# Kernel optimization log

Measured on AMD Instinct MI355X. Metric: run time of the kernel, lower is better.

The kernel has to match this reference:

```python
import jax, jax.numpy as jnp
import numpy as np

N = 8192      # number of input points
K = 16        # nsample for all kNN groupings
STRIDE = 4    # TransitionDown stride -> M = N // 4 output points


def _knn(q, p, k):
    # squared euclidean distances [m, n] -> k nearest indices per query
    d2 = jnp.sum(q * q, 1)[:, None] + jnp.sum(p * p, 1)[None, :] - 2.0 * (q @ p.T)
    return jax.lax.top_k(-d2, k)[1]


def _forward(points, We1, se1, be1, We2, se2, be2,
             Wq1, Wk1, Wv1, sa1, ba1, Wq2, Wk2, Wv2, sa2, ba2,
             Wtd, sd, bd, Wu1, su1, bu1, Wu2, su2, bu2,
             Wc1, bc1, sc, bc, Wc2, bc2):
    p = points[0]                      # [N, 3]
    n = p.shape[0]
    idx = _knn(p, p, K)                # [N, K] shared xyz-kNN (same coords every layer)

    def edge_conv(x, W, s, b):
        # DGCNN EdgeConv: concat(x_i, x_j - x_i) -> Linear -> BN(affine) -> ReLU -> max_k
        xi = x[:, None, :]
        xj = x[idx]                    # [N, K, C]
        e = jnp.concatenate([jnp.broadcast_to(xi, xj.shape), xj - xi], -1)
        h = jax.nn.relu((e @ W) * s + b)
        return h.max(axis=1)

    def graph_attn(x, Wq, Wk, Wv, s, b):
        q, kk, v = x @ Wq, x @ Wk, x @ Wv
        kj, vj = kk[idx], v[idx]       # [N, K, D]
        logits = jnp.einsum('nd,nkd->nk', q, kj) / jnp.sqrt(jnp.float32(q.shape[-1]))
        a = jax.nn.softmax(logits, axis=-1)
        y = jnp.einsum('nk,nkd->nd', a, vj)
        return jax.nn.relu(y * s + b)

    x = edge_conv(p, We1, se1, be1)            # 3 -> 64
    x = edge_conv(x, We2, se2, be2)            # 64 -> 128
    x = graph_attn(x, Wq1, Wk1, Wv1, sa1, ba1) # 128 -> 256
    x = graph_attn(x, Wq2, Wk2, Wv2, sa2, ba2) # 256 -> 512

    # TransitionDown: subsample n/stride points, group kNN with relative xyz, MLP, max-pool
    sel = jnp.arange(0, n, STRIDE)
    pm = p[sel]                                 # [M, 3]
    idx_d = _knn(pm, p, K)                      # [M, K]
    g = jnp.concatenate([p[idx_d] - pm[:, None, :], x[idx_d]], -1)  # [M, K, 3+512]
    xd = jax.nn.relu((g @ Wtd) * sd + bd).max(axis=1)               # [M, 512]

    # TransitionUp(x, o): local linear + broadcast per-cloud pooled branch (single cloud, o=[n])
    gmean = xd.mean(axis=0, keepdims=True)
    xu = jax.nn.relu((xd @ Wu1) * su1 + bu1 + (gmean @ Wu2) * su2 + bu2)  # [M, 256]

    # classifier (eval mode: dropout = identity, BN folded to affine)
    h = jax.nn.relu(((xu @ Wc1) + bc1) * sc + bc)
    return h @ Wc2 + bc2               # [M, num_classes]


def setup_inputs() -> dict:
    key = jax.random.key(0)
    ks = iter(jax.random.split(key, 64))
    def w(shape):
        return jax.random.normal(next(ks), shape, jnp.float32) / jnp.sqrt(jnp.float32(shape[0]))
    def s(d):
        return 1.0 + 0.01 * jax.random.normal(next(ks), (d,), jnp.float32)
    def b(d):
        return 0.01 * jax.random.normal(next(ks), (d,), jnp.float32)
    return {
        'points': jax.random.normal(next(ks), (1, N, 3), jnp.float32),
        'We1': w((6, 64)), 'se1': s(64), 'be1': b(64),
        'We2': w((128, 128)), 'se2': s(128), 'be2': b(128),
        'Wq1': w((128, 256)), 'Wk1': w((128, 256)), 'Wv1': w((128, 256)), 'sa1': s(256), 'ba1': b(256),
        'Wq2': w((256, 512)), 'Wk2': w((256, 512)), 'Wv2': w((256, 512)), 'sa2': s(512), 'ba2': b(512),
        'Wtd': w((515, 512)), 'sd': s(512), 'bd': b(512),
        'Wu1': w((512, 256)), 'su1': s(256), 'bu1': b(256),
        'Wu2': w((512, 256)), 'su2': s(256), 'bu2': b(256),
        'Wc1': w((256, 128)), 'bc1': b(128), 'sc': s(128), 'bc': b(128),
        'Wc2': w((128, 6)), 'bc2': b(6),
    }


def reference(points, We1, se1, be1, We2, se2, be2,
              Wq1, Wk1, Wv1, sa1, ba1, Wq2, Wk2, Wv2, sa2, ba2,
              Wtd, sd, bd, Wu1, su1, bu1, Wu2, su2, bu2,
              Wc1, bc1, sc, bc, Wc2, bc2):
    return _forward(points, We1, se1, be1, We2, se2, be2,
                    Wq1, Wk1, Wv1, sa1, ba1, Wq2, Wk2, Wv2, sa2, ba2,
                    Wtd, sd, bd, Wu1, su1, bu1, Wu2, su2, bu2,
                    Wc1, bc1, sc, bc, Wc2, bc2)
```

## Files before the change

### kernel.cpp

```cpp
#include <hip/hip_runtime.h>


#define NP 8192
#define NDOWN 2048
#define KCAP 64

typedef unsigned long long u64;
typedef __attribute__((ext_vector_type(8))) _Float16 half8;
typedef __attribute__((ext_vector_type(4))) unsigned short us4;
typedef __attribute__((ext_vector_type(8))) unsigned short ushort8;
typedef __attribute__((ext_vector_type(4))) float f32x4;

__device__ __forceinline__ bool lexless(float ad, int ai, float bd, int bi) {
  return ad < bd || (ad == bd && ai < bi);
}

__device__ __forceinline__ unsigned short f2h(float x) {
  _Float16 h = (_Float16)x;
  return __builtin_bit_cast(unsigned short, h);
}
__device__ __forceinline__ float h2f(unsigned short u) {
  return (float)__builtin_bit_cast(_Float16, u);
}

__global__ __launch_bounds__(256) void prep_points_k(const float* __restrict__ pts,
                                                     float4* __restrict__ soa) {
  int i = blockIdx.x * 256 + threadIdx.x;
  float x = pts[3 * i], y = pts[3 * i + 1], z = pts[3 * i + 2];
  soa[i] = make_float4(x, y, z, x * x + y * y + z * z);
}

__global__ __launch_bounds__(256) void wsplit_k(
    const float* __restrict__ We2, const float* __restrict__ Wq1,
    const float* __restrict__ Wk1, const float* __restrict__ Wv1,
    const float* __restrict__ Wq2, const float* __restrict__ Wk2,
    const float* __restrict__ Wv2, const float* __restrict__ Wtd,
    const float* __restrict__ Wu1, const float* __restrict__ Wc1,
    unsigned short* __restrict__ whi) {
  int t = blockIdx.x * 256 + threadIdx.x;
  float v;
  if (t < 16384) {
    int n = t >> 6, k = t & 63;
    if (n < 128) v = We2[k * 128 + n] - We2[(k + 64) * 128 + n];
    else         v = We2[(k + 64) * 128 + (n - 128)];
  } else if (t < 114688) {
    int e = t - 16384;
    int n = e >> 7, k = e & 127;
    if (n < 256)      v = Wq1[k * 256 + n];
    else if (n < 512) v = Wk1[k * 256 + (n - 256)];
    else              v = Wv1[k * 256 + (n - 512)];
  } else if (t < 507904) {
    int e = t - 114688;
    int n = e >> 8, k = e & 255;
    if (n < 512)       v = Wq2[k * 512 + n];
    else if (n < 1024) v = Wk2[k * 512 + (n - 512)];
    else               v = Wv2[k * 512 + (n - 1024)];
  } else if (t < 770048) {
    int e = t - 507904;
    int n = e >> 9, k = e & 511;
    v = Wtd[(3 + k) * 512 + n];
  } else if (t < 901120) {
    int e = t - 770048;
    int n = e >> 9, k = e & 511;
    v = Wu1[k * 256 + n];
  } else {
    int e = t - 901120;
    int n = e >> 8, k = e & 255;
    v = Wc1[k * 128 + n];
  }
  whi[t] = f2h(v);
}

__device__ __forceinline__ void bitonic_val64(float& d, int lane) {
#pragma unroll
  for (int k = 2; k <= 64; k <<= 1) {
#pragma unroll
    for (int j = k >> 1; j >= 1; j >>= 1) {
      float od = __shfl_xor(d, j);
      bool takeMin = (((lane & k) == 0) == ((lane & j) == 0));
      d = takeMin ? fminf(d, od) : fmaxf(d, od);
    }
  }
}

__device__ __forceinline__ void bitonic_lex64(float& d, int& i, int lane) {
#pragma unroll
  for (int k = 2; k <= 64; k <<= 1) {
#pragma unroll
    for (int j = k >> 1; j >= 1; j >>= 1) {
      float od = __shfl_xor(d, j);
      int oi = __shfl_xor(i, j);
      bool takeMin = (((lane & k) == 0) == ((lane & j) == 0));
      bool less = lexless(od, oi, d, i);
      if (takeMin == less) { d = od; i = oi; }
    }
  }
}

__device__ __forceinline__ void insert1(float cd, int ci, int lane,
                                        float& td, int& ti) {
  int p = __popcll(__ballot(lexless(td, ti, cd, ci)));
  if (p < 16) {
    float ud = __shfl_up(td, 1);
    int ui = __shfl_up(ti, 1);
    float ntd = td; int nti = ti;
    if (lane > p && lane < 16) { ntd = ud; nti = ui; }
    if (lane == p) { ntd = cd; nti = ci; }
    td = ntd; ti = nti;
  }
}

__global__ __launch_bounds__(512) void knn_k(const float4* __restrict__ soa,
                                             int* __restrict__ idxout) {
  __shared__ float4 sp[2048];
  __shared__ float cb_d[8][KCAP];
  __shared__ int cb_i[8][KCAP];
  __shared__ int ccnt[8];
  const int lane = threadIdx.x & 63;
  const int wid = threadIdx.x >> 6;
  const int q = blockIdx.x * 8 + wid;
  const float4 qp = soa[q];
  const float qx2 = -2.f * qp.x, qy2 = -2.f * qp.y, qz2 = -2.f * qp.z;
  const float INF = __int_as_float(0x7f800000);
  if (lane == 0) ccnt[wid] = 0;

  float md = INF;
  for (int ch = 0; ch < 4; ++ch) {
    __syncthreads();
    for (int j = 0; j < 4; ++j) {
      int e = j * 512 + threadIdx.x;
      sp[e] = soa[ch * 2048 + e];
    }
    __syncthreads();
#pragma unroll 4
    for (int c = 0; c < 32; ++c) {
      const float4 P = sp[c * 64 + lane];
      float m = fmaf(qx2, P.x, qp.w);
      m = fmaf(qy2, P.y, m);
      m = fmaf(qz2, P.z, m);
      md = fminf(md, m + P.w);
    }
  }
  float sv = md;
  bitonic_val64(sv, lane);
  const float tau = __shfl(sv, 15);
  const float tauM = tau + fabsf(tau) * 1e-5f + 1e-12f;

  for (int ch = 0; ch < 4; ++ch) {
    __syncthreads();
    for (int j = 0; j < 4; ++j) {
      int e = j * 512 + threadIdx.x;
      sp[e] = soa[ch * 2048 + e];
    }
    __syncthreads();
#pragma unroll 4
    for (int c = 0; c < 32; ++c) {
      const float4 P = sp[c * 64 + lane];
      float m = fmaf(qx2, P.x, qp.w);
      m = fmaf(qy2, P.y, m);
      m = fmaf(qz2, P.z, m);
      const float d = m + P.w;
      if (d <= tauM) {
        int slot = atomicAdd(&ccnt[wid], 1);
        if (slot < KCAP) {
          cb_d[wid][slot] = d;
          cb_i[wid][slot] = ch * 2048 + c * 64 + lane;
        }
      }
    }
  }
  int n = ccnt[wid];
  if (n <= KCAP) {
    float dd = (lane < n) ? cb_d[wid][lane] : INF;
    int ii = (lane < n) ? cb_i[wid][lane] : 0x7fffffff;
    bitonic_lex64(dd, ii, lane);
    if (lane < 16) idxout[q * 16 + lane] = ii & 8191;
  } else {
    float td = INF; int ti = 0x7fffffff;
    float Td = INF; int Ti = 0x7fffffff;
    for (int base = 0; base < 8192; base += 64) {
      const float4 P = soa[base + lane];
      float m = fmaf(qx2, P.x, qp.w);
      m = fmaf(qy2, P.y, m);
      m = fmaf(qz2, P.z, m);
      const float d = m + P.w;
      const int gidx = base + lane;
      u64 mk = __ballot(d <= tauM && lexless(d, gidx, Td, Ti));
      while (mk) {
        int s = (int)__builtin_ctzll(mk);
        mk &= mk - 1;
        float cd = __shfl(d, s);
        int ci = __shfl(gidx, s);
        insert1(cd, ci, lane, td, ti);
      }
      Td = __shfl(td, 15); Ti = __shfl(ti, 15);
    }
    if (lane < 16) idxout[q * 16 + lane] = ti & 8191;
  }
}

__global__ __launch_bounds__(256) void proj1_k(const float4* __restrict__ soa,
                                               const float* __restrict__ We1,
                                               float* __restrict__ bz1) {
  int t = blockIdx.x * 256 + threadIdx.x;
  int i = t >> 7, c = t & 127;
  float4 P = soa[i];
  float v;
  if (c < 64) {
    v = P.x * (We1[c] - We1[192 + c]) + P.y * (We1[64 + c] - We1[256 + c]) +
        P.z * (We1[128 + c] - We1[320 + c]);
  } else {
    int cc = c & 63;
    v = P.x * We1[192 + cc] + P.y * We1[256 + cc] + P.z * We1[320 + cc];
  }
  bz1[t] = v;
}

template <int C>
__global__ __launch_bounds__(256) void ec_gm_k(const float* __restrict__ bz,
                                               const int* __restrict__ idx,
                                               const float* __restrict__ s,
                                               const float* __restrict__ b,
                                               unsigned short* __restrict__ xo) {
  constexpr int C4 = C / 4;
  int t = blockIdx.x * 256 + threadIdx.x;
  int i = t / C4, q = t % C4;
  float4 base = *(const float4*)&bz[(size_t)i * (2 * C) + q * 4];
  float4 scl = *(const float4*)&s[q * 4];
  float4 bia = *(const float4*)&b[q * 4];
  float ax = 0.f, ay = 0.f, az = 0.f, aw = 0.f;
  const int* ip = idx + i * 16;
#pragma unroll
  for (int n = 0; n < 16; ++n) {
    int j = ip[n];
    float4 z = *(const float4*)&bz[(size_t)j * (2 * C) + C + q * 4];
    ax = fmaxf(ax, (base.x + z.x) * scl.x + bia.x);
    ay = fmaxf(ay, (base.y + z.y) * scl.y + bia.y);
    az = fmaxf(az, (base.z + z.z) * scl.z + bia.z);
    aw = fmaxf(aw, (base.w + z.w) * scl.w + bia.w);
  }
  us4 o;
  o[0] = f2h(ax); o[1] = f2h(ay); o[2] = f2h(az); o[3] = f2h(aw);
  *(us4*)&xo[(size_t)i * C + q * 4] = o;
}

template <int C>
__global__ __launch_bounds__(256) void attn_fused_k(const float* __restrict__ qf,
                                                    const unsigned short* __restrict__ kvb,
                                                    const int* __restrict__ idx,
                                                    const float* __restrict__ s,
                                                    const float* __restrict__ b,
                                                    unsigned short* __restrict__ xo,
                                                    float scale) {
  int i = blockIdx.x * 4 + (threadIdx.x >> 6);
  int lane = threadIdx.x & 63;
  constexpr int G = C / 256;
  int jreg = (lane < 16) ? idx[i * 16 + lane] : 0;
  float4 qv[G];
#pragma unroll
  for (int g = 0; g < G; ++g)
    qv[g] = *(const float4*)&qf[(size_t)i * C + 4 * lane + 256 * g];
  float lg[16];
#pragma unroll
  for (int n = 0; n < 16; ++n) {
    int j = __shfl(jreg, n);
    const unsigned short* kr = kvb + (size_t)j * (2 * C);
    float ssum = 0.f;
#pragma unroll
    for (int g = 0; g < G; ++g) {
      us4 kk = *(const us4*)&kr[4 * lane + 256 * g];
      ssum += qv[g].x * h2f(kk[0]) + qv[g].y * h2f(kk[1]) +
              qv[g].z * h2f(kk[2]) + qv[g].w * h2f(kk[3]);
    }
    lg[n] = ssum;
  }
#pragma unroll
  for (int n = 0; n < 16; ++n) {
    float vv = lg[n];
    for (int o = 32; o >= 1; o >>= 1) vv += __shfl_xor(vv, o);
    lg[n] = vv * scale;
  }
  float m = lg[0];
#pragma unroll
  for (int n = 1; n < 16; ++n) m = fmaxf(m, lg[n]);
  float ssum = 0.f;
#pragma unroll
  for (int n = 0; n < 16; ++n) { lg[n] = __expf(lg[n] - m); ssum += lg[n]; }
  float inv = 1.f / ssum;
#pragma unroll
  for (int n = 0; n < 16; ++n) lg[n] *= inv;

  float acc[4 * G];
#pragma unroll
  for (int e = 0; e < 4 * G; ++e) acc[e] = 0.f;
#pragma unroll
  for (int n = 0; n < 16; ++n) {
    int j = __shfl(jreg, n);
    const unsigned short* vr = kvb + (size_t)j * (2 * C) + C;
    float w = lg[n];
#pragma unroll
    for (int g = 0; g < G; ++g) {
      us4 v4 = *(const us4*)&vr[4 * lane + 256 * g];
      acc[4 * g + 0] += w * h2f(v4[0]);
      acc[4 * g + 1] += w * h2f(v4[1]);
      acc[4 * g + 2] += w * h2f(v4[2]);
      acc[4 * g + 3] += w * h2f(v4[3]);
    }
  }
#pragma unroll
  for (int g = 0; g < G; ++g) {
    int c0 = 4 * lane + 256 * g;
    float4 scl = *(const float4*)&s[c0];
    float4 bia = *(const float4*)&b[c0];
    us4 o;
    o[0] = f2h(fmaxf(acc[4 * g + 0] * scl.x + bia.x, 0.f));
    o[1] = f2h(fmaxf(acc[4 * g + 1] * scl.y + bia.y, 0.f));
    o[2] = f2h(fmaxf(acc[4 * g + 2] * scl.z + bia.z, 0.f));
    o[3] = f2h(fmaxf(acc[4 * g + 3] * scl.w + bia.w, 0.f));
    *(us4*)&xo[(size_t)i * C + c0] = o;
  }
}

__global__ __launch_bounds__(256) void down_gm_k(const float* __restrict__ vbuf,
                                                 const float4* __restrict__ soa,
                                                 const float* __restrict__ Wtd,
                                                 const int* __restrict__ idx,
                                                 const float* __restrict__ sd,
                                                 const float* __restrict__ bd,
                                                 unsigned short* __restrict__ xd) {
  int t = blockIdx.x * 256 + threadIdx.x;
  int i = t >> 7, q = t & 127;
  int qi = 4 * i;
  float4 qp = soa[qi];
  float4 w0 = *(const float4*)&Wtd[q * 4];
  float4 w1 = *(const float4*)&Wtd[512 + q * 4];
  float4 w2 = *(const float4*)&Wtd[1024 + q * 4];
  float px = qp.x * w0.x + qp.y * w1.x + qp.z * w2.x;
  float py = qp.x * w0.y + qp.y * w1.y + qp.z * w2.y;
  float pz = qp.x * w0.z + qp.y * w1.z + qp.z * w2.z;
  float pw2 = qp.x * w0.w + qp.y * w1.w + qp.z * w2.w;
  float4 scl = *(const float4*)&sd[q * 4];
  float4 bia = *(const float4*)&bd[q * 4];
  float ax = 0.f, ay = 0.f, az = 0.f, aw = 0.f;
  const int* ip = idx + qi * 16;
#pragma unroll
  for (int n = 0; n < 16; ++n) {
    int j = ip[n];
    float4 v = *(const float4*)&vbuf[(size_t)j * 512 + q * 4];
    ax = fmaxf(ax, (v.x - px) * scl.x + bia.x);
    ay = fmaxf(ay, (v.y - py) * scl.y + bia.y);
    az = fmaxf(az, (v.z - pz) * scl.z + bia.z);
    aw = fmaxf(aw, (v.w - pw2) * scl.w + bia.w);
  }
  us4 o;
  o[0] = f2h(ax); o[1] = f2h(ay); o[2] = f2h(az); o[3] = f2h(aw);
  *(us4*)&xd[(size_t)i * 512 + q * 4] = o;
}

__global__ __launch_bounds__(512) void colsum_k(const unsigned short* __restrict__ xd,
                                                float* __restrict__ part) {
  int b = blockIdx.x;
  int c = threadIdx.x;
  float s = 0.f;
  for (int r = b * 128; r < (b + 1) * 128; ++r) s += h2f(xd[(size_t)r * 512 + c]);
  part[b * 512 + c] = s;
}

__global__ __launch_bounds__(256) void gterm_k(const float* __restrict__ part,
                                               const float* __restrict__ Wu2,
                                               const float* __restrict__ su2,
                                               const float* __restrict__ bu2,
                                               float* __restrict__ gterm) {
  __shared__ float gm[512];
  int tid = threadIdx.x;
  for (int c = tid; c < 512; c += 256) {
    float s = 0.f;
#pragma unroll
    for (int b = 0; b < 16; ++b) s += part[b * 512 + c];
    gm[c] = s * (1.f / 2048.f);
  }
  __syncthreads();
  int o = blockIdx.x * 16 + (tid >> 4);
  int kseg = tid & 15;
  float s = 0.f;
#pragma unroll 8
  for (int k = kseg * 32; k < kseg * 32 + 32; ++k) s += gm[k] * Wu2[k * 256 + o];
  s += __shfl_xor(s, 1);
  s += __shfl_xor(s, 2);
  s += __shfl_xor(s, 4);
  s += __shfl_xor(s, 8);
  if (kseg == 0) gterm[o] = s * su2[o] + bu2[o];
}

#define LDSROW 80
template <int MODE>
__global__ __launch_bounds__(256) void gemm_mfma(
    const unsigned short* __restrict__ A,
    const unsigned short* __restrict__ B,
    float* __restrict__ Cf, unsigned short* __restrict__ Ch,
    int M, int N, int K,
    const float4* __restrict__ soaD, const float* __restrict__ wtd,
    const float* __restrict__ s1, const float* __restrict__ b1,
    const float* __restrict__ s2, int Cq, unsigned short* __restrict__ kvb) {
  __shared__ __align__(16) char smem[2 * 128 * LDSROW];
  char* A_s = smem;
  char* B_s = smem + 128 * LDSROW;

  const int tid = threadIdx.x;
  const int lane = tid & 63;
  const int wid = tid >> 6;
  const int wm = wid >> 1, wn = wid & 1;
  const int bm = blockIdx.y * 128, bn = blockIdx.x * 128;
  const int r16 = lane & 15, kb = lane >> 4;

  f32x4 acc[4][4];
#pragma unroll
  for (int a = 0; a < 4; ++a)
#pragma unroll
    for (int b = 0; b < 4; ++b) acc[a][b] = (f32x4)(0.f);

  for (int k0 = 0; k0 < K; k0 += 32) {
    __syncthreads();
#pragma unroll
    for (int qq = 0; qq < 2; ++qq) {
      int idx8 = qq * 256 + tid;
      int row = idx8 >> 2, sq = idx8 & 3;
      size_t goA = (size_t)(bm + row) * K + k0 + sq * 8;
      size_t goB = (size_t)(bn + row) * K + k0 + sq * 8;
      ushort8 a_v = *(const ushort8*)&A[goA];
      ushort8 b_v = *(const ushort8*)&B[goB];
      *(ushort8*)(A_s + row * LDSROW + sq * 16) = a_v;
      *(ushort8*)(B_s + row * LDSROW + sq * 16) = b_v;
    }
    __syncthreads();

    half8 ah[4];
#pragma unroll
    for (int mi = 0; mi < 4; ++mi) {
      int off = (wm * 64 + mi * 16 + r16) * LDSROW + kb * 16;
      ah[mi] = *(const half8*)(A_s + off);
    }
#pragma unroll
    for (int ni = 0; ni < 4; ++ni) {
      int off = (wn * 64 + ni * 16 + r16) * LDSROW + kb * 16;
      half8 bh = *(const half8*)(B_s + off);
#pragma unroll
      for (int mi = 0; mi < 4; ++mi) {
        acc[mi][ni] = __builtin_amdgcn_mfma_f32_16x16x32_f16(ah[mi], bh, acc[mi][ni], 0, 0, 0);
      }
    }
  }

#pragma unroll
  for (int mi = 0; mi < 4; ++mi) {
#pragma unroll
    for (int ni = 0; ni < 4; ++ni) {
      int r0 = bm + wm * 64 + mi * 16 + (lane >> 4) * 4;
      int cc = bn + wn * 64 + ni * 16 + (lane & 15);
      float w0 = 0.f, w1 = 0.f, w2 = 0.f;
      if (MODE == 1) { w0 = wtd[cc]; w1 = wtd[512 + cc]; w2 = wtd[1024 + cc]; }
#pragma unroll
      for (int j = 0; j < 4; ++j) {
        float vv = acc[mi][ni][j];
        int row = r0 + j;
        if (MODE == 1) {
          float4 P = soaD[row];
          vv += P.x * w0 + P.y * w1 + P.z * w2;
        }
        if (MODE == 2) vv = fmaxf(vv * s1[cc] + b1[cc] + s2[cc], 0.f);
        if (MODE == 3) vv = fmaxf((vv + b1[cc]) * s1[cc] + s2[cc], 0.f);
        if (MODE == 2) {
          Ch[(size_t)row * N + cc] = f2h(vv);
        } else if (MODE == 4) {
          if (cc < Cq) Cf[(size_t)row * Cq + cc] = vv;
          else kvb[(size_t)row * (2 * Cq) + (cc - Cq)] = f2h(vv);
        } else {
          Cf[(size_t)row * N + cc] = vv;
        }
      }
    }
  }
}

__global__ __launch_bounds__(256) void out_k(const float* __restrict__ h,
                                             const float* __restrict__ Wc2,
                                             const float* __restrict__ bc2,
                                             float* __restrict__ out) {
  int t = blockIdx.x * 256 + threadIdx.x;
  int pair = t >> 2, kq = t & 3;
  int i = pair / 6, o = pair % 6;
  float s = 0.f;
#pragma unroll 8
  for (int m = kq * 32; m < kq * 32 + 32; ++m) s += h[i * 128 + m] * Wc2[m * 6 + o];
  s += __shfl_xor(s, 1);
  s += __shfl_xor(s, 2);
  if (kq == 0) out[pair] = s + bc2[o];
}

extern "C" void kernel_launch(void* const* d_in, const int* in_sizes, int n_in,
                              void* d_out, int out_size, void* d_ws, size_t ws_size,
                              hipStream_t stream) {
  const float* pts = (const float*)d_in[0];
  const float* We1 = (const float*)d_in[1];
  const float* se1 = (const float*)d_in[2];
  const float* be1 = (const float*)d_in[3];
  const float* We2 = (const float*)d_in[4];
  const float* se2 = (const float*)d_in[5];
  const float* be2 = (const float*)d_in[6];
  const float* Wq1 = (const float*)d_in[7];
  const float* Wk1 = (const float*)d_in[8];
  const float* Wv1 = (const float*)d_in[9];
  const float* sa1 = (const float*)d_in[10];
  const float* ba1 = (const float*)d_in[11];
  const float* Wq2 = (const float*)d_in[12];
  const float* Wk2 = (const float*)d_in[13];
  const float* Wv2 = (const float*)d_in[14];
  const float* sa2 = (const float*)d_in[15];
  const float* ba2 = (const float*)d_in[16];
  const float* Wtd = (const float*)d_in[17];
  const float* sd  = (const float*)d_in[18];
  const float* bd  = (const float*)d_in[19];
  const float* Wu1 = (const float*)d_in[20];
  const float* su1 = (const float*)d_in[21];
  const float* bu1 = (const float*)d_in[22];
  const float* Wu2 = (const float*)d_in[23];
  const float* su2 = (const float*)d_in[24];
  const float* bu2 = (const float*)d_in[25];
  const float* Wc1 = (const float*)d_in[26];
  const float* bc1 = (const float*)d_in[27];
  const float* sc  = (const float*)d_in[28];
  const float* bc  = (const float*)d_in[29];
  const float* Wc2 = (const float*)d_in[30];
  const float* bc2 = (const float*)d_in[31];

  float* ws = (float*)d_ws;
  if (ws_size < (size_t)16703744 * 4) return;
  float* soa   = ws;
  int*   idx   = (int*)(ws + 32768);
  float* gpart = ws + 294912;
  float* gterm = ws + 303104;
  unsigned short* wthi = (unsigned short*)(ws + 303360);
  unsigned short* x1   = (unsigned short*)(ws + 1237248);
  unsigned short* x2   = (unsigned short*)(ws + 1499392);
  unsigned short* x3   = (unsigned short*)(ws + 2023680);
  unsigned short* x4   = (unsigned short*)(ws + 3072256);
  unsigned short* xd   = (unsigned short*)(ws + 5169408);
  unsigned short* xu   = (unsigned short*)(ws + 5693696);
  float* bufP  = ws + 5955840;
  float* qf    = ws + 8052992;
  unsigned short* kvb = (unsigned short*)(ws + 12247296);
  float* hbuf  = ws + 16441600;

  prep_points_k<<<32, 256, 0, stream>>>(pts, (float4*)soa);
  wsplit_k<<<3648, 256, 0, stream>>>(We2, Wq1, Wk1, Wv1, Wq2, Wk2, Wv2, Wtd, Wu1, Wc1, wthi);
  knn_k<<<1024, 512, 0, stream>>>((const float4*)soa, idx);

  proj1_k<<<4096, 256, 0, stream>>>((const float4*)soa, We1, bufP);
  ec_gm_k<64><<<512, 256, 0, stream>>>(bufP, idx, se1, be1, x1);

  gemm_mfma<0><<<dim3(2, 64), 256, 0, stream>>>(x1, wthi,
      bufP, nullptr, NP, 256, 64, nullptr, nullptr, nullptr, nullptr, nullptr, 0, nullptr);
  ec_gm_k<128><<<1024, 256, 0, stream>>>(bufP, idx, se2, be2, x2);

  gemm_mfma<4><<<dim3(6, 64), 256, 0, stream>>>(x2, wthi + 16384,
      qf, nullptr, NP, 768, 128, nullptr, nullptr, nullptr, nullptr, nullptr, 256, kvb);
  attn_fused_k<256><<<2048, 256, 0, stream>>>(qf, kvb, idx, sa1, ba1, x3, 0.0625f);

  gemm_mfma<4><<<dim3(12, 64), 256, 0, stream>>>(x3, wthi + 114688,
      qf, nullptr, NP, 1536, 256, nullptr, nullptr, nullptr, nullptr, nullptr, 512, kvb);
  attn_fused_k<512><<<2048, 256, 0, stream>>>(qf, kvb, idx, sa2, ba2, x4, 0.04419417382415922f);

  gemm_mfma<1><<<dim3(4, 64), 256, 0, stream>>>(x4, wthi + 507904,
      qf, nullptr, NP, 512, 512, (const float4*)soa, Wtd, nullptr, nullptr, nullptr, 0, nullptr);
  down_gm_k<<<1024, 256, 0, stream>>>(qf, (const float4*)soa, Wtd, idx, sd, bd, xd);

  colsum_k<<<16, 512, 0, stream>>>(xd, gpart);
  gterm_k<<<16, 256, 0, stream>>>(gpart, Wu2, su2, bu2, gterm);

  gemm_mfma<2><<<dim3(2, 16), 256, 0, stream>>>(xd, wthi + 770048,
      nullptr, xu, NDOWN, 256, 512, nullptr, nullptr, su1, bu1, gterm, 0, nullptr);
  gemm_mfma<3><<<dim3(1, 16), 256, 0, stream>>>(xu, wthi + 901120,
      hbuf, nullptr, NDOWN, 128, 256, nullptr, nullptr, sc, bc1, bc, 0, nullptr);
  out_k<<<192, 256, 0, stream>>>(hbuf, Wc2, bc2, (float*)d_out);
}
```

Before: 266.6 us.

## Batch kNN queries per wave, halve intermediates to fp16, widen GEMM N tiles

The kNN kernel now handles four queries per wave. It builds an exact top-16 seed from each lane's nearest point and then filters the remaining candidates through a smaller buffer with sequential insertion. The two point-prep kernels are merged into one launch. Intermediate projection buffers (EdgeConv pre-activations, TransitionDown values) are stored in fp16 instead of fp32 to halve gather traffic. The GEMM is templated on N-fragment count so blocks cover 256 columns, which halves grid size and raises per-wave reuse, at the cost of more registers and possible fp16 rounding differences.

```diff
diff --git a/kernel.cpp b/kernel.cpp
--- a/kernel.cpp
+++ b/kernel.cpp
@@ -3,7 +3,7 @@
 
 #define NP 8192
 #define NDOWN 2048
-#define KCAP 64
+#define KCAP 24
 
 typedef unsigned long long u64;
 typedef __attribute__((ext_vector_type(8))) _Float16 half8;
@@ -23,21 +23,22 @@
   return (float)__builtin_bit_cast(_Float16, u);
 }
 
-__global__ __launch_bounds__(256) void prep_points_k(const float* __restrict__ pts,
-                                                     float4* __restrict__ soa) {
-  int i = blockIdx.x * 256 + threadIdx.x;
-  float x = pts[3 * i], y = pts[3 * i + 1], z = pts[3 * i + 2];
-  soa[i] = make_float4(x, y, z, x * x + y * y + z * z);
-}
-
-__global__ __launch_bounds__(256) void wsplit_k(
+__global__ __launch_bounds__(256) void prep_all_k(
+    const float* __restrict__ pts, float4* __restrict__ soa,
     const float* __restrict__ We2, const float* __restrict__ Wq1,
     const float* __restrict__ Wk1, const float* __restrict__ Wv1,
     const float* __restrict__ Wq2, const float* __restrict__ Wk2,
     const float* __restrict__ Wv2, const float* __restrict__ Wtd,
     const float* __restrict__ Wu1, const float* __restrict__ Wc1,
     unsigned short* __restrict__ whi) {
-  int t = blockIdx.x * 256 + threadIdx.x;
+  int blk = blockIdx.x;
+  if (blk < 32) {
+    int i = blk * 256 + threadIdx.x;
+    float x = pts[3 * i], y = pts[3 * i + 1], z = pts[3 * i + 2];
+    soa[i] = make_float4(x, y, z, x * x + y * y + z * z);
+    return;
+  }
+  int t = (blk - 32) * 256 + threadIdx.x;
   float v;
   if (t < 16384) {
     int n = t >> 6, k = t & 63;
@@ -71,18 +72,6 @@
   whi[t] = f2h(v);
 }
 
-__device__ __forceinline__ void bitonic_val64(float& d, int lane) {
-#pragma unroll
-  for (int k = 2; k <= 64; k <<= 1) {
-#pragma unroll
-    for (int j = k >> 1; j >= 1; j >>= 1) {
-      float od = __shfl_xor(d, j);
-      bool takeMin = (((lane & k) == 0) == ((lane & j) == 0));
-      d = takeMin ? fminf(d, od) : fmaxf(d, od);
-    }
-  }
-}
-
 __device__ __forceinline__ void bitonic_lex64(float& d, int& i, int lane) {
 #pragma unroll
   for (int k = 2; k <= 64; k <<= 1) {
@@ -113,18 +102,25 @@
 __global__ __launch_bounds__(512) void knn_k(const float4* __restrict__ soa,
                                              int* __restrict__ idxout) {
   __shared__ float4 sp[2048];
-  __shared__ float cb_d[8][KCAP];
-  __shared__ int cb_i[8][KCAP];
-  __shared__ int ccnt[8];
+  __shared__ float cb_d[32][KCAP];
+  __shared__ int cb_i[32][KCAP];
+  __shared__ int ccnt[32];
   const int lane = threadIdx.x & 63;
   const int wid = threadIdx.x >> 6;
-  const int q = blockIdx.x * 8 + wid;
-  const float4 qp = soa[q];
-  const float qx2 = -2.f * qp.x, qy2 = -2.f * qp.y, qz2 = -2.f * qp.z;
+  const int q0 = blockIdx.x * 32 + wid * 4;
   const float INF = __int_as_float(0x7f800000);
-  if (lane == 0) ccnt[wid] = 0;
-
-  float md = INF;
+  float qx2[4], qy2[4], qz2[4], qw[4];
+#pragma unroll
+  for (int qi = 0; qi < 4; ++qi) {
+    float4 qp = soa[q0 + qi];
+    qx2[qi] = -2.f * qp.x; qy2[qi] = -2.f * qp.y; qz2[qi] = -2.f * qp.z;
+    qw[qi] = qp.w;
+  }
+  if (lane < 4) ccnt[wid * 4 + lane] = 0;
+
+  float md[4]; int mi[4];
+#pragma unroll
+  for (int qi = 0; qi < 4; ++qi) { md[qi] = INF; mi[qi] = 0x7fffffff; }
   for (int ch = 0; ch < 4; ++ch) {
     __syncthreads();
     for (int j = 0; j < 4; ++j) {
@@ -135,16 +131,30 @@
 #pragma unroll 4
     for (int c = 0; c < 32; ++c) {
       const float4 P = sp[c * 64 + lane];
-      float m = fmaf(qx2, P.x, qp.w);
-      m = fmaf(qy2, P.y, m);
-      m = fmaf(qz2, P.z, m);
-      md = fminf(md, m + P.w);
-    }
-  }
-  float sv = md;
-  bitonic_val64(sv, lane);
-  const float tau = __shfl(sv, 15);
-  const float tauM = tau + fabsf(tau) * 1e-5f + 1e-12f;
+      const int gidx = ch * 2048 + c * 64 + lane;
+#pragma unroll
+      for (int qi = 0; qi < 4; ++qi) {
+        float d = fmaf(qx2[qi], P.x, qw[qi]);
+        d = fmaf(qy2[qi], P.y, d);
+        d = fmaf(qz2[qi], P.z, d);
+        d += P.w;
+        if (d < md[qi]) { md[qi] = d; mi[qi] = gidx; }
+      }
+    }
+  }
+  int own[4];
+  float td[4], Td[4], tau[4];
+  int ti[4], Ti[4];
+#pragma unroll
+  for (int qi = 0; qi < 4; ++qi) {
+    own[qi] = mi[qi];
+    float sd = md[qi]; int si = mi[qi];
+    bitonic_lex64(sd, si, lane);
+    td[qi] = (lane < 16) ? sd : INF;
+    ti[qi] = (lane < 16) ? si : 0x7fffffff;
+    Td[qi] = __shfl(sd, 15); Ti[qi] = __shfl(si, 15);
+    tau[qi] = Td[qi] + fabsf(Td[qi]) * 1e-5f + 1e-12f;
+  }
 
   for (int ch = 0; ch < 4; ++ch) {
     __syncthreads();
@@ -156,68 +166,85 @@
 #pragma unroll 4
     for (int c = 0; c < 32; ++c) {
       const float4 P = sp[c * 64 + lane];
-      float m = fmaf(qx2, P.x, qp.w);
-      m = fmaf(qy2, P.y, m);
-      m = fmaf(qz2, P.z, m);
-      const float d = m + P.w;
-      if (d <= tauM) {
-        int slot = atomicAdd(&ccnt[wid], 1);
-        if (slot < KCAP) {
-          cb_d[wid][slot] = d;
-          cb_i[wid][slot] = ch * 2048 + c * 64 + lane;
+      const int gidx = ch * 2048 + c * 64 + lane;
+#pragma unroll
+      for (int qi = 0; qi < 4; ++qi) {
+        float d = fmaf(qx2[qi], P.x, qw[qi]);
+        d = fmaf(qy2[qi], P.y, d);
+        d = fmaf(qz2[qi], P.z, d);
+        d += P.w;
+        if (d <= tau[qi] && gidx != own[qi]) {
+          int slot = atomicAdd(&ccnt[wid * 4 + qi], 1);
+          if (slot < KCAP) {
+            cb_d[wid * 4 + qi][slot] = d;
+            cb_i[wid * 4 + qi][slot] = gidx;
+          }
         }
       }
     }
   }
-  int n = ccnt[wid];
-  if (n <= KCAP) {
-    float dd = (lane < n) ? cb_d[wid][lane] : INF;
-    int ii = (lane < n) ? cb_i[wid][lane] : 0x7fffffff;
-    bitonic_lex64(dd, ii, lane);
-    if (lane < 16) idxout[q * 16 + lane] = ii & 8191;
-  } else {
-    float td = INF; int ti = 0x7fffffff;
-    float Td = INF; int Ti = 0x7fffffff;
-    for (int base = 0; base < 8192; base += 64) {
-      const float4 P = soa[base + lane];
-      float m = fmaf(qx2, P.x, qp.w);
-      m = fmaf(qy2, P.y, m);
-      m = fmaf(qz2, P.z, m);
-      const float d = m + P.w;
-      const int gidx = base + lane;
-      u64 mk = __ballot(d <= tauM && lexless(d, gidx, Td, Ti));
-      while (mk) {
-        int s = (int)__builtin_ctzll(mk);
-        mk &= mk - 1;
-        float cd = __shfl(d, s);
-        int ci = __shfl(gidx, s);
-        insert1(cd, ci, lane, td, ti);
+
+#pragma unroll
+  for (int qi = 0; qi < 4; ++qi) {
+    int n = ccnt[wid * 4 + qi];
+    if (n <= KCAP) {
+      for (int k2 = 0; k2 < n; ++k2) {
+        float cd = cb_d[wid * 4 + qi][k2];
+        int ci = cb_i[wid * 4 + qi][k2];
+        if (lexless(cd, ci, Td[qi], Ti[qi])) {
+          insert1(cd, ci, lane, td[qi], ti[qi]);
+          Td[qi] = __shfl(td[qi], 15); Ti[qi] = __shfl(ti[qi], 15);
+        }
       }
-      Td = __shfl(td, 15); Ti = __shfl(ti, 15);
-    }
-    if (lane < 16) idxout[q * 16 + lane] = ti & 8191;
+    } else {
+      td[qi] = INF; ti[qi] = 0x7fffffff; Td[qi] = INF; Ti[qi] = 0x7fffffff;
+      for (int base = 0; base < 8192; base += 64) {
+        const float4 P = soa[base + lane];
+        float d = fmaf(qx2[qi], P.x, qw[qi]);
+        d = fmaf(qy2[qi], P.y, d);
+        d = fmaf(qz2[qi], P.z, d);
+        d += P.w;
+        const int gidx = base + lane;
+        u64 mk = __ballot(d <= tau[qi] && lexless(d, gidx, Td[qi], Ti[qi]));
+        while (mk) {
+          int s = (int)__builtin_ctzll(mk);
+          mk &= mk - 1;
+          float cd = __shfl(d, s);
+          int ci = __shfl(gidx, s);
+          insert1(cd, ci, lane, td[qi], ti[qi]);
+        }
+        Td[qi] = __shfl(td[qi], 15); Ti[qi] = __shfl(ti[qi], 15);
+      }
+    }
+    if (lane < 16) idxout[(q0 + qi) * 16 + lane] = ti[qi] & 8191;
   }
 }
 
 __global__ __launch_bounds__(256) void proj1_k(const float4* __restrict__ soa,
                                                const float* __restrict__ We1,
-                                               float* __restrict__ bz1) {
+                                               unsigned short* __restrict__ bz1) {
   int t = blockIdx.x * 256 + threadIdx.x;
-  int i = t >> 7, c = t & 127;
+  int i = t >> 5, g = t & 31;
   float4 P = soa[i];
-  float v;
-  if (c < 64) {
-    v = P.x * (We1[c] - We1[192 + c]) + P.y * (We1[64 + c] - We1[256 + c]) +
-        P.z * (We1[128 + c] - We1[320 + c]);
-  } else {
-    int cc = c & 63;
-    v = P.x * We1[192 + cc] + P.y * We1[256 + cc] + P.z * We1[320 + cc];
-  }
-  bz1[t] = v;
+  us4 o;
+#pragma unroll
+  for (int j = 0; j < 4; ++j) {
+    int c = 4 * g + j;
+    float v;
+    if (c < 64) {
+      v = P.x * (We1[c] - We1[192 + c]) + P.y * (We1[64 + c] - We1[256 + c]) +
+          P.z * (We1[128 + c] - We1[320 + c]);
+    } else {
+      int cc = c & 63;
+      v = P.x * We1[192 + cc] + P.y * We1[256 + cc] + P.z * We1[320 + cc];
+    }
+    o[j] = f2h(v);
+  }
+  *(us4*)&bz1[(size_t)i * 128 + 4 * g] = o;
 }
 
 template <int C>
-__global__ __launch_bounds__(256) void ec_gm_k(const float* __restrict__ bz,
+__global__ __launch_bounds__(256) void ec_gm_k(const unsigned short* __restrict__ bz,
                                                const int* __restrict__ idx,
                                                const float* __restrict__ s,
                                                const float* __restrict__ b,
@@ -225,7 +252,8 @@
   constexpr int C4 = C / 4;
   int t = blockIdx.x * 256 + threadIdx.x;
   int i = t / C4, q = t % C4;
-  float4 base = *(const float4*)&bz[(size_t)i * (2 * C) + q * 4];
+  us4 b4 = *(const us4*)&bz[(size_t)i * (2 * C) + q * 4];
+  float bx = h2f(b4[0]), by = h2f(b4[1]), bz2v = h2f(b4[2]), bw = h2f(b4[3]);
   float4 scl = *(const float4*)&s[q * 4];
   float4 bia = *(const float4*)&b[q * 4];
   float ax = 0.f, ay = 0.f, az = 0.f, aw = 0.f;
@@ -233,11 +261,11 @@
 #pragma unroll
   for (int n = 0; n < 16; ++n) {
     int j = ip[n];
-    float4 z = *(const float4*)&bz[(size_t)j * (2 * C) + C + q * 4];
-    ax = fmaxf(ax, (base.x + z.x) * scl.x + bia.x);
-    ay = fmaxf(ay, (base.y + z.y) * scl.y + bia.y);
-    az = fmaxf(az, (base.z + z.z) * scl.z + bia.z);
-    aw = fmaxf(aw, (base.w + z.w) * scl.w + bia.w);
+    us4 z4 = *(const us4*)&bz[(size_t)j * (2 * C) + C + q * 4];
+    ax = fmaxf(ax, (bx + h2f(z4[0])) * scl.x + bia.x);
+    ay = fmaxf(ay, (by + h2f(z4[1])) * scl.y + bia.y);
+    az = fmaxf(az, (bz2v + h2f(z4[2])) * scl.z + bia.z);
+    aw = fmaxf(aw, (bw + h2f(z4[3])) * scl.w + bia.w);
   }
   us4 o;
   o[0] = f2h(ax); o[1] = f2h(ay); o[2] = f2h(az); o[3] = f2h(aw);
@@ -321,7 +349,7 @@
   }
 }
 
-__global__ __launch_bounds__(256) void down_gm_k(const float* __restrict__ vbuf,
+__global__ __launch_bounds__(256) void down_gm_k(const unsigned short* __restrict__ vbuf,
                                                  const float4* __restrict__ soa,
                                                  const float* __restrict__ Wtd,
                                                  const int* __restrict__ idx,
@@ -346,11 +374,11 @@
 #pragma unroll
   for (int n = 0; n < 16; ++n) {
     int j = ip[n];
-    float4 v = *(const float4*)&vbuf[(size_t)j * 512 + q * 4];
-    ax = fmaxf(ax, (v.x - px) * scl.x + bia.x);
-    ay = fmaxf(ay, (v.y - py) * scl.y + bia.y);
-    az = fmaxf(az, (v.z - pz) * scl.z + bia.z);
-    aw = fmaxf(aw, (v.w - pw2) * scl.w + bia.w);
+    us4 v4 = *(const us4*)&vbuf[(size_t)j * 512 + q * 4];
+    ax = fmaxf(ax, (h2f(v4[0]) - px) * scl.x + bia.x);
+    ay = fmaxf(ay, (h2f(v4[1]) - py) * scl.y + bia.y);
+    az = fmaxf(az, (h2f(v4[2]) - pz) * scl.z + bia.z);
+    aw = fmaxf(aw, (h2f(v4[3]) - pw2) * scl.w + bia.w);
   }
   us4 o;
   o[0] = f2h(ax); o[1] = f2h(ay); o[2] = f2h(az); o[3] = f2h(aw);
@@ -392,8 +420,7 @@
   if (kseg == 0) gterm[o] = s * su2[o] + bu2[o];
 }
 
-#define LDSROW 80
-template <int MODE>
+template <int MODE, int NFR>
 __global__ __launch_bounds__(256) void gemm_mfma(
     const unsigned short* __restrict__ A,
     const unsigned short* __restrict__ B,
@@ -402,22 +429,23 @@
     const float4* __restrict__ soaD, const float* __restrict__ wtd,
     const float* __restrict__ s1, const float* __restrict__ b1,
     const float* __restrict__ s2, int Cq, unsigned short* __restrict__ kvb) {
-  __shared__ __align__(16) char smem[2 * 128 * LDSROW];
+  constexpr int BROWS = NFR * 32;
+  __shared__ __align__(16) char smem[(128 + BROWS) * 80];
   char* A_s = smem;
-  char* B_s = smem + 128 * LDSROW;
+  char* B_s = smem + 128 * 80;
 
   const int tid = threadIdx.x;
   const int lane = tid & 63;
   const int wid = tid >> 6;
   const int wm = wid >> 1, wn = wid & 1;
-  const int bm = blockIdx.y * 128, bn = blockIdx.x * 128;
+  const int bm = blockIdx.y * 128, bn = blockIdx.x * BROWS;
   const int r16 = lane & 15, kb = lane >> 4;
 
-  f32x4 acc[4][4];
+  f32x4 acc[4][NFR];
 #pragma unroll
   for (int a = 0; a < 4; ++a)
 #pragma unroll
-    for (int b = 0; b < 4; ++b) acc[a][b] = (f32x4)(0.f);
+    for (int b = 0; b < NFR; ++b) acc[a][b] = (f32x4)(0.f);
 
   for (int k0 = 0; k0 < K; k0 += 32) {
     __syncthreads();
@@ -425,24 +453,27 @@
     for (int qq = 0; qq < 2; ++qq) {
       int idx8 = qq * 256 + tid;
       int row = idx8 >> 2, sq = idx8 & 3;
-      size_t goA = (size_t)(bm + row) * K + k0 + sq * 8;
-      size_t goB = (size_t)(bn + row) * K + k0 + sq * 8;
-      ushort8 a_v = *(const ushort8*)&A[goA];
-      ushort8 b_v = *(const ushort8*)&B[goB];
-      *(ushort8*)(A_s + row * LDSROW + sq * 16) = a_v;
-      *(ushort8*)(B_s + row * LDSROW + sq * 16) = b_v;
+      ushort8 a_v = *(const ushort8*)&A[(size_t)(bm + row) * K + k0 + sq * 8];
+      *(ushort8*)(A_s + row * 80 + sq * 16) = a_v;
+    }
+#pragma unroll
+    for (int qq = 0; qq < NFR / 2; ++qq) {
+      int idx8 = qq * 256 + tid;
+      int row = idx8 >> 2, sq = idx8 & 3;
+      ushort8 b_v = *(const ushort8*)&B[(size_t)(bn + row) * K + k0 + sq * 8];
+      *(ushort8*)(B_s + row * 80 + sq * 16) = b_v;
     }
     __syncthreads();
 
     half8 ah[4];
 #pragma unroll
     for (int mi = 0; mi < 4; ++mi) {
-      int off = (wm * 64 + mi * 16 + r16) * LDSROW + kb * 16;
+      int off = (wm * 64 + mi * 16 + r16) * 80 + kb * 16;
       ah[mi] = *(const half8*)(A_s + off);
     }
 #pragma unroll
-    for (int ni = 0; ni < 4; ++ni) {
-      int off = (wn * 64 + ni * 16 + r16) * LDSROW + kb * 16;
+    for (int ni = 0; ni < NFR; ++ni) {
+      int off = (wn * NFR * 16 + ni * 16 + r16) * 80 + kb * 16;
       half8 bh = *(const half8*)(B_s + off);
 #pragma unroll
       for (int mi = 0; mi < 4; ++mi) {
@@ -454,9 +485,9 @@
 #pragma unroll
   for (int mi = 0; mi < 4; ++mi) {
 #pragma unroll
-    for (int ni = 0; ni < 4; ++ni) {
+    for (int ni = 0; ni < NFR; ++ni) {
       int r0 = bm + wm * 64 + mi * 16 + (lane >> 4) * 4;
-      int cc = bn + wn * 64 + ni * 16 + (lane & 15);
+      int cc = bn + wn * NFR * 16 + ni * 16 + (lane & 15);
       float w0 = 0.f, w1 = 0.f, w2 = 0.f;
       if (MODE == 1) { w0 = wtd[cc]; w1 = wtd[512 + cc]; w2 = wtd[1024 + cc]; }
 #pragma unroll
@@ -469,7 +500,7 @@
         }
         if (MODE == 2) vv = fmaxf(vv * s1[cc] + b1[cc] + s2[cc], 0.f);
         if (MODE == 3) vv = fmaxf((vv + b1[cc]) * s1[cc] + s2[cc], 0.f);
-        if (MODE == 2) {
+        if (MODE == 0 || MODE == 1 || MODE == 2) {
           Ch[(size_t)row * N + cc] = f2h(vv);
         } else if (MODE == 4) {
           if (cc < Cq) Cf[(size_t)row * Cq + cc] = vv;
@@ -546,40 +577,41 @@
   unsigned short* x4   = (unsigned short*)(ws + 3072256);
   unsigned short* xd   = (unsigned short*)(ws + 5169408);
   unsigned short* xu   = (unsigned short*)(ws + 5693696);
-  float* bufP  = ws + 5955840;
+  unsigned short* bzb  = (unsigned short*)(ws + 5955840);
   float* qf    = ws + 8052992;
+  unsigned short* vbuf = (unsigned short*)qf;
   unsigned short* kvb = (unsigned short*)(ws + 12247296);
   float* hbuf  = ws + 16441600;
 
-  prep_points_k<<<32, 256, 0, stream>>>(pts, (float4*)soa);
-  wsplit_k<<<3648, 256, 0, stream>>>(We2, Wq1, Wk1, Wv1, Wq2, Wk2, Wv2, Wtd, Wu1, Wc1, wthi);
-  knn_k<<<1024, 512, 0, stream>>>((const float4*)soa, idx);
-
-  proj1_k<<<4096, 256, 0, stream>>>((const float4*)soa, We1, bufP);
-  ec_gm_k<64><<<512, 256, 0, stream>>>(bufP, idx, se1, be1, x1);
-
-  gemm_mfma<0><<<dim3(2, 64), 256, 0, stream>>>(x1, wthi,
-      bufP, nullptr, NP, 256, 64, nullptr, nullptr, nullptr, nullptr, nullptr, 0, nullptr);
-  ec_gm_k<128><<<1024, 256, 0, stream>>>(bufP, idx, se2, be2, x2);
-
-  gemm_mfma<4><<<dim3(6, 64), 256, 0, stream>>>(x2, wthi + 16384,
+  prep_all_k<<<3680, 256, 0, stream>>>(pts, (float4*)soa, We2, Wq1, Wk1, Wv1,
+                                       Wq2, Wk2, Wv2, Wtd, Wu1, Wc1, wthi);
+  knn_k<<<256, 512, 0, stream>>>((const float4*)soa, idx);
+
+  proj1_k<<<1024, 256, 0, stream>>>((const float4*)soa, We1, bzb);
+  ec_gm_k<64><<<512, 256, 0, stream>>>(bzb, idx, se1, be1, x1);
+
+  gemm_mfma<0, 8><<<dim3(1, 64), 256, 0, stream>>>(x1, wthi,
+      nullptr, bzb, NP, 256, 64, nullptr, nullptr, nullptr, nullptr, nullptr, 0, nullptr);
+  ec_gm_k<128><<<1024, 256, 0, stream>>>(bzb, idx, se2, be2, x2);
+
+  gemm_mfma<4, 8><<<dim3(3, 64), 256, 0, stream>>>(x2, wthi + 16384,
       qf, nullptr, NP, 768, 128, nullptr, nullptr, nullptr, nullptr, nullptr, 256, kvb);
   attn_fused_k<256><<<2048, 256, 0, stream>>>(qf, kvb, idx, sa1, ba1, x3, 0.0625f);
 
-  gemm_mfma<4><<<dim3(12, 64), 256, 0, stream>>>(x3, wthi + 114688,
+  gemm_mfma<4, 8><<<dim3(6, 64), 256, 0, stream>>>(x3, wthi + 114688,
       qf, nullptr, NP, 1536, 256, nullptr, nullptr, nullptr, nullptr, nullptr, 512, kvb);
   attn_fused_k<512><<<2048, 256, 0, stream>>>(qf, kvb, idx, sa2, ba2, x4, 0.04419417382415922f);
 
-  gemm_mfma<1><<<dim3(4, 64), 256, 0, stream>>>(x4, wthi + 507904,
-      qf, nullptr, NP, 512, 512, (const float4*)soa, Wtd, nullptr, nullptr, nullptr, 0, nullptr);
-  down_gm_k<<<1024, 256, 0, stream>>>(qf, (const float4*)soa, Wtd, idx, sd, bd, xd);
+  gemm_mfma<1, 8><<<dim3(2, 64), 256, 0, stream>>>(x4, wthi + 507904,
+      nullptr, vbuf, NP, 512, 512, (const float4*)soa, Wtd, nullptr, nullptr, nullptr, 0, nullptr);
+  down_gm_k<<<1024, 256, 0, stream>>>(vbuf, (const float4*)soa, Wtd, idx, sd, bd, xd);
 
   colsum_k<<<16, 512, 0, stream>>>(xd, gpart);
   gterm_k<<<16, 256, 0, stream>>>(gpart, Wu2, su2, bu2, gterm);
 
-  gemm_mfma<2><<<dim3(2, 16), 256, 0, stream>>>(xd, wthi + 770048,
+  gemm_mfma<2, 8><<<dim3(1, 16), 256, 0, stream>>>(xd, wthi + 770048,
       nullptr, xu, NDOWN, 256, 512, nullptr, nullptr, su1, bu1, gterm, 0, nullptr);
-  gemm_mfma<3><<<dim3(1, 16), 256, 0, stream>>>(xu, wthi + 901120,
+  gemm_mfma<3, 4><<<dim3(1, 16), 256, 0, stream>>>(xu, wthi + 901120,
       hbuf, nullptr, NDOWN, 128, 256, nullptr, nullptr, sc, bc1, bc, 0, nullptr);
   out_k<<<192, 256, 0, stream>>>(hbuf, Wc2, bc2, (float*)d_out);
 }
```

Result: slower. 285.8 us (+7.2%).
